# Kernel optimization log

Measured on AMD Instinct MI355X. Metric: run time of the kernel, lower is better.

## Reference

```python
import jax, jax.numpy as jnp
import numpy as np

B, S, D, H = 2, 2048, 1024, 16
DK = D // H


def setup_inputs() -> dict:
    key = jax.random.key(0)
    ks = jax.random.split(key, 11)
    scale = jnp.float32(1.0 / np.sqrt(D))
    inp = {
        "query": jax.random.normal(ks[0], (B, S, D), jnp.float32),
        "key": jax.random.normal(ks[1], (B, S, D), jnp.float32),
        "value": jax.random.normal(ks[2], (B, S, D), jnp.float32),
        # causal mask: True = masked (masked_fill semantics), broadcast over batch/heads
        "mask": jnp.triu(jnp.ones((S, S), dtype=bool), k=1)[None, None, :, :],
        "Wq": jax.random.normal(ks[3], (D, D), jnp.float32) * scale,
        "bq": jnp.zeros((D,), jnp.float32),
        "Wk": jax.random.normal(ks[4], (D, D), jnp.float32) * scale,
        "bk": jnp.zeros((D,), jnp.float32),
        "Wv": jax.random.normal(ks[5], (D, D), jnp.float32) * scale,
        "bv": jnp.zeros((D,), jnp.float32),
        "Wo": jax.random.normal(ks[6], (D, D), jnp.float32) * scale,
        "bo": jnp.zeros((D,), jnp.float32),
    }
    return inp


def _split_heads(x):
    # (B, S, D) -> (B, H, S, DK)
    b, s, _ = x.shape
    return x.reshape(b, s, H, DK).transpose(0, 2, 1, 3)


def reference(query, key, value, mask, Wq, bq, Wk, bk, Wv, bv, Wo, bo):
    # nn.Linear: y = x @ W.T + b
    q = _split_heads(query @ Wq.T + bq)
    k = _split_heads(key @ Wk.T + bk)
    v = _split_heads(value @ Wv.T + bv)

    inv_sqrt_dk = jnp.float32(1.0 / np.sqrt(DK))
    scores = jnp.einsum("bhqd,bhkd->bhqk", q, k) * inv_sqrt_dk  # (B,H,S,S)
    scores = jnp.where(mask, jnp.float32(-jnp.inf), scores)
    weights = jax.nn.softmax(scores, axis=-1)
    weights = jnp.nan_to_num(weights, nan=0.0)  # fully-masked rows -> 0

    attn = jnp.einsum("bhqk,bhkd->bhqd", weights, v)  # (B,H,S,DK)
    merged = attn.transpose(0, 2, 1, 3).reshape(B, S, D)  # merge heads
    return merged @ Wo.T + bo
```

## Files before the change

kernel.cpp:

```cpp
#include <hip/hip_runtime.h>


typedef unsigned short u16;
typedef unsigned int u32;
typedef __attribute__((ext_vector_type(8))) __bf16 bf16x8;
typedef __attribute__((ext_vector_type(8))) unsigned short us8;
typedef __attribute__((ext_vector_type(4))) unsigned short us4;
typedef __attribute__((ext_vector_type(4))) unsigned int u32x4;
typedef __attribute__((ext_vector_type(4))) float f32x4;

#define S_LEN 2048
#define D_DIM 1024
#define NH 16
#define DKH 64
#define Mi 1048576ULL

__device__ __forceinline__ u16 f2bf(float f) {
  return __builtin_bit_cast(u16, (__bf16)f);
}
__device__ __forceinline__ u32 pack2(float lo, float hi) {
  return (u32)f2bf(lo) | ((u32)f2bf(hi) << 16);
}
__device__ __forceinline__ bf16x8 ld_frag(const u16* p) {
  us8 v = *(const us8*)p;
  return __builtin_bit_cast(bf16x8, v);
}
__device__ __forceinline__ void gl2lds16(const u16* g, u16* l) {
  __builtin_amdgcn_global_load_lds(
      (__attribute__((address_space(1))) void*)(g),
      (__attribute__((address_space(3))) void*)(l), 16, 0, 0);
}
__device__ __forceinline__ void stage_f32(const float* __restrict__ g, int ld,
                                          u16* lds, int t) {
  int row = t >> 1, col = (t & 1) * 16;
  const float* p = g + (size_t)row * ld + col;
  us8 o0, o1;
  #pragma unroll
  for (int i = 0; i < 8; ++i) o0[i] = f2bf(p[i]);
  #pragma unroll
  for (int i = 0; i < 8; ++i) o1[i] = f2bf(p[8 + i]);
  *(us8*)&lds[row * 32 + col] = o0;
  *(us8*)&lds[row * 32 + col + 8] = o1;
}

__global__ __launch_bounds__(256, 1) void cvt_all(
    const float* __restrict__ q, const float* __restrict__ k, const float* __restrict__ v,
    const float* __restrict__ wq, const float* __restrict__ wk,
    const float* __restrict__ wv, const float* __restrict__ wo,
    u16* __restrict__ dst)
{
  size_t e0 = ((size_t)blockIdx.x * 256 + threadIdx.x) * 8;
  const float* s;
  if      (e0 <  4*Mi) s = q  + e0;
  else if (e0 <  8*Mi) s = k  + (e0 - 4*Mi);
  else if (e0 < 12*Mi) s = v  + (e0 - 8*Mi);
  else if (e0 < 13*Mi) s = wq + (e0 - 12*Mi);
  else if (e0 < 14*Mi) s = wk + (e0 - 13*Mi);
  else if (e0 < 15*Mi) s = wv + (e0 - 14*Mi);
  else                 s = wo + (e0 - 15*Mi);
  float4 a = ((const float4*)s)[0];
  float4 b = ((const float4*)s)[1];
  us8 o;
  o[0]=f2bf(a.x); o[1]=f2bf(a.y); o[2]=f2bf(a.z); o[3]=f2bf(a.w);
  o[4]=f2bf(b.x); o[5]=f2bf(b.y); o[6]=f2bf(b.z); o[7]=f2bf(b.w);
  *(us8*)(dst + e0) = o;
}

__global__ __launch_bounds__(256, 1) void gemm_qkv_bb(
    const u16* __restrict__ Aq, const u16* __restrict__ Ak, const u16* __restrict__ Av,
    const u16* __restrict__ Wqb, const u16* __restrict__ Wkb, const u16* __restrict__ Wvb,
    const float* __restrict__ bq, const float* __restrict__ bk, const float* __restrict__ bv,
    u16* __restrict__ Oq, u16* __restrict__ Ok, u16* __restrict__ Ov, float qscale)
{
  const int z = blockIdx.z;
  const u16* A = (z == 0) ? Aq : (z == 1) ? Ak : Av;
  const u16* W = (z == 0) ? Wqb : (z == 1) ? Wkb : Wvb;
  const float* bias = (z == 0) ? bq : (z == 1) ? bk : bv;
  u16* out = (z == 0) ? Oq : (z == 1) ? Ok : Ov;
  const float scale = (z == 0) ? qscale : 1.0f;
  const int K = 1024;

  __shared__ u16 lA[128 * 32];
  __shared__ u16 lB[128 * 32];
  const int t = threadIdx.x;
  const int w = t >> 6, l = t & 63;
  const int mblk = blockIdx.y * 128, nblk = blockIdx.x * 128;
  const int wm = (w & 1) * 64, wn = (w >> 1) * 64;
  const int lr = l & 15, lq = l >> 4;
  const int srow = l >> 2, scol = (l & 3) * 8;

  f32x4 acc[4][4] = {};

  for (int k0 = 0; k0 < K; k0 += 32) {
    __syncthreads();
    #pragma unroll
    for (int r = 0; r < 2; ++r) {
      int grp = r * 4 + w;
      gl2lds16(A + (size_t)(mblk + grp * 16 + srow) * K + k0 + scol, &lA[grp * 512]);
      gl2lds16(W + (size_t)(nblk + grp * 16 + srow) * K + k0 + scol, &lB[grp * 512]);
    }
    __syncthreads();
    bf16x8 aF[4], bF[4];
    #pragma unroll
    for (int mt = 0; mt < 4; ++mt)
      aF[mt] = ld_frag(&lA[(wm + mt * 16 + lr) * 32 + lq * 8]);
    #pragma unroll
    for (int nt = 0; nt < 4; ++nt)
      bF[nt] = ld_frag(&lB[(wn + nt * 16 + lr) * 32 + lq * 8]);
    #pragma unroll
    for (int mt = 0; mt < 4; ++mt)
      #pragma unroll
      for (int nt = 0; nt < 4; ++nt)
        acc[mt][nt] = __builtin_amdgcn_mfma_f32_16x16x32_bf16(aF[mt], bF[nt], acc[mt][nt], 0, 0, 0);
  }

  #pragma unroll
  for (int mt = 0; mt < 4; ++mt)
    #pragma unroll
    for (int nt = 0; nt < 4; ++nt)
      #pragma unroll
      for (int r = 0; r < 4; ++r) {
        int rowg = mblk + wm + mt * 16 + lq * 4 + r;
        int colg = nblk + wn + nt * 16 + lr;
        float v = (acc[mt][nt][r] + bias[colg]) * scale;
        int b = rowg >> 11, s = rowg & 2047;
        int h = colg >> 6, dk = colg & 63;
        if (z != 2)
          out[(((size_t)(b * NH + h)) * S_LEN + s) * DKH + dk] = f2bf(v);
        else
          out[(((size_t)(b * NH + h)) * DKH + dk) * S_LEN + s] = f2bf(v);
      }
}

__global__ __launch_bounds__(256, 1) void gemm_out_bb(
    const u16* __restrict__ A, const u16* __restrict__ W,
    const float* __restrict__ bias, float* __restrict__ out)
{
  const int K = 1024;
  __shared__ u16 lA[128 * 32];
  __shared__ u16 lB[128 * 32];
  const int t = threadIdx.x;
  const int w = t >> 6, l = t & 63;
  const int mblk = blockIdx.y * 128, nblk = blockIdx.x * 128;
  const int wm = (w & 1) * 64, wn = (w >> 1) * 64;
  const int lr = l & 15, lq = l >> 4;
  const int srow = l >> 2, scol = (l & 3) * 8;

  f32x4 acc[4][4] = {};

  for (int k0 = 0; k0 < K; k0 += 32) {
    __syncthreads();
    #pragma unroll
    for (int r = 0; r < 2; ++r) {
      int grp = r * 4 + w;
      gl2lds16(A + (size_t)(mblk + grp * 16 + srow) * K + k0 + scol, &lA[grp * 512]);
      gl2lds16(W + (size_t)(nblk + grp * 16 + srow) * K + k0 + scol, &lB[grp * 512]);
    }
    __syncthreads();
    bf16x8 aF[4], bF[4];
    #pragma unroll
    for (int mt = 0; mt < 4; ++mt)
      aF[mt] = ld_frag(&lA[(wm + mt * 16 + lr) * 32 + lq * 8]);
    #pragma unroll
    for (int nt = 0; nt < 4; ++nt)
      bF[nt] = ld_frag(&lB[(wn + nt * 16 + lr) * 32 + lq * 8]);
    #pragma unroll
    for (int mt = 0; mt < 4; ++mt)
      #pragma unroll
      for (int nt = 0; nt < 4; ++nt)
        acc[mt][nt] = __builtin_amdgcn_mfma_f32_16x16x32_bf16(aF[mt], bF[nt], acc[mt][nt], 0, 0, 0);
  }

  #pragma unroll
  for (int mt = 0; mt < 4; ++mt)
    #pragma unroll
    for (int nt = 0; nt < 4; ++nt)
      #pragma unroll
      for (int r = 0; r < 4; ++r) {
        int rowg = mblk + wm + mt * 16 + lq * 4 + r;
        int colg = nblk + wn + nt * 16 + lr;
        out[(size_t)rowg * D_DIM + colg] = acc[mt][nt][r] + bias[colg];
      }
}

__global__ __launch_bounds__(256, 1) void attn_fused(
    const u16* __restrict__ Q, const u16* __restrict__ K,
    const u16* __restrict__ Vt, u16* __restrict__ O)
{
  __shared__ u16 lK[2][64 * 64];
  __shared__ u16 lV[2][64 * 64];
  __shared__ u32 lPT[4 * 16 * 32];

  const int idx = blockIdx.x;
  const int s_ = idx >> 8;
  const int r_ = idx & 255;
  const int bh = r_ & 31;
  const int t_ = r_ >> 5;
  const int qt = (s_ == 0) ? t_ : (s_ == 1) ? 31 - t_ : (s_ == 2) ? 8 + t_ : 23 - t_;
  const int b = bh >> 4, h = bh & 15;
  const int t = threadIdx.x;
  const int w = t >> 6, l = t & 63;
  const int lr = l & 15, lq = l >> 4;

  const u16* Qp = Q + (size_t)bh * S_LEN * DKH;
  const u16* Kp = K + (size_t)bh * S_LEN * DKH;
  const u16* Vp = Vt + (size_t)bh * DKH * S_LEN;

  const int srow8 = l >> 3;
  const int schunk = l & 7;

  const int qrow = qt * 64 + w * 16 + lr;
  bf16x8 qf[2];
  qf[0] = ld_frag(Qp + (size_t)qrow * DKH + lq * 8);
  qf[1] = ld_frag(Qp + (size_t)qrow * DKH + 32 + lq * 8);

  f32x4 o[4] = {};
  f32x4 li4 = {};

  u32* pw = &lPT[w * 16 * 32];
  const int pswz = (lr & 7) << 2;

  #pragma unroll
  for (int r2 = 0; r2 < 2; ++r2) {
    int grp = r2 * 4 + w;
    int row = grp * 8 + srow8;
    int c = schunk ^ (row & 7);
    gl2lds16(Kp + (size_t)row * DKH + c * 8, &lK[0][grp * 512]);
    gl2lds16(Vp + (size_t)row * S_LEN + c * 8, &lV[0][grp * 512]);
  }

  for (int kt = 0; kt <= qt; ++kt) {
    const int cur = kt & 1;
    __syncthreads();

    if (kt < qt) {
      #pragma unroll
      for (int r2 = 0; r2 < 2; ++r2) {
        int grp = r2 * 4 + w;
        int row = grp * 8 + srow8;
        int c = schunk ^ (row & 7);
        gl2lds16(Kp + (size_t)((kt + 1) * 64 + row) * DKH + c * 8, &lK[cur ^ 1][grp * 512]);
        gl2lds16(Vp + (size_t)row * S_LEN + (kt + 1) * 64 + c * 8, &lV[cur ^ 1][grp * 512]);
      }
    }

    f32x4 st[4] = {};
    #pragma unroll
    for (int ks = 0; ks < 2; ++ks)
      #pragma unroll
      for (int nt = 0; nt < 4; ++nt) {
        int row = nt * 16 + lr;
        int cs = (ks * 4 + lq) ^ (row & 7);
        bf16x8 kb = ld_frag(&lK[cur][row * 64 + cs * 8]);
        st[nt] = __builtin_amdgcn_mfma_f32_16x16x32_bf16(kb, qf[ks], st[nt], 0, 0, 0);
      }

    float p[4][4];
    const bool diag = (kt == qt);
    const int qloc = w * 16 + lr;
    #pragma unroll
    for (int nt = 0; nt < 4; ++nt) {
      #pragma unroll
      for (int r = 0; r < 4; ++r) {
        int kk = nt * 16 + lq * 4 + r;
        float e = exp2f(st[nt][r]);
        p[nt][r] = (diag && kk > qloc) ? 0.0f : e;
        li4[r] += p[nt][r];
      }
    }

    #pragma unroll
    for (int nt = 0; nt < 4; ++nt) {
      #pragma unroll
      for (int i = 0; i < 2; ++i) {
        int pr = nt * 8 + lq * 2 + i;
        pw[lr * 32 + (pr ^ pswz)] = pack2(p[nt][2 * i], p[nt][2 * i + 1]);
      }
    }
    #pragma unroll
    for (int ks = 0; ks < 2; ++ks) {
      u32x4 pv;
      #pragma unroll
      for (int u = 0; u < 4; ++u) {
        int pr = ks * 16 + lq * 4 + u;
        pv[u] = pw[lr * 32 + (pr ^ pswz)];
      }
      bf16x8 pb = __builtin_bit_cast(bf16x8, pv);
      #pragma unroll
      for (int nt = 0; nt < 4; ++nt) {
        int vrow = nt * 16 + lr;
        int vcs = (ks * 4 + lq) ^ (vrow & 7);
        bf16x8 vb = ld_frag(&lV[cur][vrow * 64 + vcs * 8]);
        o[nt] = __builtin_amdgcn_mfma_f32_16x16x32_bf16(vb, pb, o[nt], 0, 0, 0);
      }
    }
  }

  float li = li4[0] + li4[1] + li4[2] + li4[3];
  li += __shfl_xor(li, 16);
  li += __shfl_xor(li, 32);
  const float rinv = 1.0f / li;

  const size_t orow = ((size_t)b * S_LEN + qt * 64 + w * 16 + lr) * D_DIM + h * DKH;
  #pragma unroll
  for (int nt = 0; nt < 4; ++nt) {
    us4 pk;
    #pragma unroll
    for (int r = 0; r < 4; ++r) pk[r] = f2bf(o[nt][r] * rinv);
    *(us4*)(O + orow + nt * 16 + lq * 4) = pk;
  }
}

extern "C" void kernel_launch(void* const* d_in, const int* in_sizes, int n_in,
                              void* d_out, int out_size, void* d_ws, size_t ws_size,
                              hipStream_t stream) {
  const float* query = (const float*)d_in[0];
  const float* key   = (const float*)d_in[1];
  const float* value = (const float*)d_in[2];
  const float* Wq = (const float*)d_in[4];
  const float* bq = (const float*)d_in[5];
  const float* Wk = (const float*)d_in[6];
  const float* bk = (const float*)d_in[7];
  const float* Wv = (const float*)d_in[8];
  const float* bv = (const float*)d_in[9];
  const float* Wo = (const float*)d_in[10];
  const float* bo = (const float*)d_in[11];
  float* out = (float*)d_out;

  const float qscale = 0.125f * 1.44269504088896341f;
  dim3 blk(256);

  u16* base = (u16*)d_ws;
  u16* Qb = base;
  u16* Kb = base + 4 * Mi;
  u16* Vb = base + 8 * Mi;

  u16* cvt = base + 12 * Mi;
  u16* qbf = cvt;
  u16* kbf = cvt + 4 * Mi;
  u16* vbf = cvt + 8 * Mi;
  u16* wqb = cvt + 12 * Mi;
  u16* wkb = cvt + 13 * Mi;
  u16* wvb = cvt + 14 * Mi;
  u16* wob = cvt + 15 * Mi;
  u16* Ab  = qbf;

  cvt_all<<<dim3(8192), blk, 0, stream>>>(query, key, value, Wq, Wk, Wv, Wo, cvt);
  gemm_qkv_bb<<<dim3(8, 32, 3), blk, 0, stream>>>(qbf, kbf, vbf, wqb, wkb, wvb,
                                                  bq, bk, bv, Qb, Kb, Vb, qscale);
  attn_fused<<<dim3(1024), blk, 0, stream>>>(Qb, Kb, Vb, Ab);
  gemm_out_bb<<<dim3(8, 32), blk, 0, stream>>>(Ab, wob, bo, out);
}
```

Before: 239.5 us.

## Keep softmax probabilities in registers via permuted K rows; narrow output GEMM tiles

The attention kernel permutes which K rows each lane reads, so the score MFMA output already matches the A-operand layout needed for the P·V MFMA. This removes the per-tile round trip of probabilities through shared memory, and the swizzle pattern is changed to match the new access order. The output projection GEMM moves to 128x64 tiles, doubling the grid to 512 blocks for better CU occupancy on the 1024-wide output, at the cost of more reloads of the A operand. The attention output is now written as scattered 2-byte stores instead of 8-byte vector stores, which may reduce store efficiency.

```diff
diff --git a/kernel.cpp b/kernel.cpp
--- a/kernel.cpp
+++ b/kernel.cpp
@@ -5,8 +5,6 @@
 typedef unsigned int u32;
 typedef __attribute__((ext_vector_type(8))) __bf16 bf16x8;
 typedef __attribute__((ext_vector_type(8))) unsigned short us8;
-typedef __attribute__((ext_vector_type(4))) unsigned short us4;
-typedef __attribute__((ext_vector_type(4))) unsigned int u32x4;
 typedef __attribute__((ext_vector_type(4))) float f32x4;
 
 #define S_LEN 2048
@@ -18,9 +16,6 @@
 __device__ __forceinline__ u16 f2bf(float f) {
   return __builtin_bit_cast(u16, (__bf16)f);
 }
-__device__ __forceinline__ u32 pack2(float lo, float hi) {
-  return (u32)f2bf(lo) | ((u32)f2bf(hi) << 16);
-}
 __device__ __forceinline__ bf16x8 ld_frag(const u16* p) {
   us8 v = *(const us8*)p;
   return __builtin_bit_cast(bf16x8, v);
@@ -29,18 +24,6 @@
   __builtin_amdgcn_global_load_lds(
       (__attribute__((address_space(1))) void*)(g),
       (__attribute__((address_space(3))) void*)(l), 16, 0, 0);
-}
-__device__ __forceinline__ void stage_f32(const float* __restrict__ g, int ld,
-                                          u16* lds, int t) {
-  int row = t >> 1, col = (t & 1) * 16;
-  const float* p = g + (size_t)row * ld + col;
-  us8 o0, o1;
-  #pragma unroll
-  for (int i = 0; i < 8; ++i) o0[i] = f2bf(p[i]);
-  #pragma unroll
-  for (int i = 0; i < 8; ++i) o1[i] = f2bf(p[8 + i]);
-  *(us8*)&lds[row * 32 + col] = o0;
-  *(us8*)&lds[row * 32 + col + 8] = o1;
 }
 
 __global__ __launch_bounds__(256, 1) void cvt_all(
@@ -138,15 +121,15 @@
 {
   const int K = 1024;
   __shared__ u16 lA[128 * 32];
-  __shared__ u16 lB[128 * 32];
+  __shared__ u16 lB[64 * 32];
   const int t = threadIdx.x;
   const int w = t >> 6, l = t & 63;
-  const int mblk = blockIdx.y * 128, nblk = blockIdx.x * 128;
-  const int wm = (w & 1) * 64, wn = (w >> 1) * 64;
+  const int mblk = blockIdx.y * 128, nblk = blockIdx.x * 64;
+  const int wm = (w & 1) * 64, wn = (w >> 1) * 32;
   const int lr = l & 15, lq = l >> 4;
   const int srow = l >> 2, scol = (l & 3) * 8;
 
-  f32x4 acc[4][4] = {};
+  f32x4 acc[4][2] = {};
 
   for (int k0 = 0; k0 < K; k0 += 32) {
     __syncthreads();
@@ -154,27 +137,27 @@
     for (int r = 0; r < 2; ++r) {
       int grp = r * 4 + w;
       gl2lds16(A + (size_t)(mblk + grp * 16 + srow) * K + k0 + scol, &lA[grp * 512]);
-      gl2lds16(W + (size_t)(nblk + grp * 16 + srow) * K + k0 + scol, &lB[grp * 512]);
     }
-    __syncthreads();
-    bf16x8 aF[4], bF[4];
+    gl2lds16(W + (size_t)(nblk + w * 16 + srow) * K + k0 + scol, &lB[w * 512]);
+    __syncthreads();
+    bf16x8 aF[4], bF[2];
     #pragma unroll
     for (int mt = 0; mt < 4; ++mt)
       aF[mt] = ld_frag(&lA[(wm + mt * 16 + lr) * 32 + lq * 8]);
     #pragma unroll
-    for (int nt = 0; nt < 4; ++nt)
+    for (int nt = 0; nt < 2; ++nt)
       bF[nt] = ld_frag(&lB[(wn + nt * 16 + lr) * 32 + lq * 8]);
     #pragma unroll
     for (int mt = 0; mt < 4; ++mt)
       #pragma unroll
-      for (int nt = 0; nt < 4; ++nt)
+      for (int nt = 0; nt < 2; ++nt)
         acc[mt][nt] = __builtin_amdgcn_mfma_f32_16x16x32_bf16(aF[mt], bF[nt], acc[mt][nt], 0, 0, 0);
   }
 
   #pragma unroll
   for (int mt = 0; mt < 4; ++mt)
     #pragma unroll
-    for (int nt = 0; nt < 4; ++nt)
+    for (int nt = 0; nt < 2; ++nt)
       #pragma unroll
       for (int r = 0; r < 4; ++r) {
         int rowg = mblk + wm + mt * 16 + lq * 4 + r;
@@ -189,7 +172,6 @@
 {
   __shared__ u16 lK[2][64 * 64];
   __shared__ u16 lV[2][64 * 64];
-  __shared__ u32 lPT[4 * 16 * 32];
 
   const int idx = blockIdx.x;
   const int s_ = idx >> 8;
@@ -217,14 +199,12 @@
   f32x4 o[4] = {};
   f32x4 li4 = {};
 
-  u32* pw = &lPT[w * 16 * 32];
-  const int pswz = (lr & 7) << 2;
-
   #pragma unroll
   for (int r2 = 0; r2 < 2; ++r2) {
     int grp = r2 * 4 + w;
     int row = grp * 8 + srow8;
-    int c = schunk ^ (row & 7);
+    int sw = (row & 3) | (((row >> 3) & 1) << 2);
+    int c = schunk ^ sw;
     gl2lds16(Kp + (size_t)row * DKH + c * 8, &lK[0][grp * 512]);
     gl2lds16(Vp + (size_t)row * S_LEN + c * 8, &lV[0][grp * 512]);
   }
@@ -238,7 +218,8 @@
       for (int r2 = 0; r2 < 2; ++r2) {
         int grp = r2 * 4 + w;
         int row = grp * 8 + srow8;
-        int c = schunk ^ (row & 7);
+        int sw = (row & 3) | (((row >> 3) & 1) << 2);
+        int c = schunk ^ sw;
         gl2lds16(Kp + (size_t)((kt + 1) * 64 + row) * DKH + c * 8, &lK[cur ^ 1][grp * 512]);
         gl2lds16(Vp + (size_t)row * S_LEN + (kt + 1) * 64 + c * 8, &lV[cur ^ 1][grp * 512]);
       }
@@ -246,52 +227,44 @@
 
     f32x4 st[4] = {};
     #pragma unroll
-    for (int ks = 0; ks < 2; ++ks)
+    for (int ksd = 0; ksd < 2; ++ksd)
       #pragma unroll
       for (int nt = 0; nt < 4; ++nt) {
-        int row = nt * 16 + lr;
-        int cs = (ks * 4 + lq) ^ (row & 7);
-        bf16x8 kb = ld_frag(&lK[cur][row * 64 + cs * 8]);
-        st[nt] = __builtin_amdgcn_mfma_f32_16x16x32_bf16(kb, qf[ks], st[nt], 0, 0, 0);
+        int sig = 32 * (nt >> 1) + 8 * (lr >> 2) + 4 * (nt & 1) + (lr & 3);
+        int slot = (ksd * 4 + lq) ^ (lr & 7);
+        bf16x8 kb = ld_frag(&lK[cur][sig * 64 + slot * 8]);
+        st[nt] = __builtin_amdgcn_mfma_f32_16x16x32_bf16(kb, qf[ksd], st[nt], 0, 0, 0);
       }
 
     float p[4][4];
     const bool diag = (kt == qt);
     const int qloc = w * 16 + lr;
     #pragma unroll
-    for (int nt = 0; nt < 4; ++nt) {
+    for (int nt = 0; nt < 4; ++nt)
       #pragma unroll
       for (int r = 0; r < 4; ++r) {
-        int kk = nt * 16 + lq * 4 + r;
+        int kk = 32 * (nt >> 1) + 8 * lq + 4 * (nt & 1) + r;
         float e = exp2f(st[nt][r]);
         p[nt][r] = (diag && kk > qloc) ? 0.0f : e;
         li4[r] += p[nt][r];
       }
-    }
-
-    #pragma unroll
-    for (int nt = 0; nt < 4; ++nt) {
-      #pragma unroll
-      for (int i = 0; i < 2; ++i) {
-        int pr = nt * 8 + lq * 2 + i;
-        pw[lr * 32 + (pr ^ pswz)] = pack2(p[nt][2 * i], p[nt][2 * i + 1]);
-      }
-    }
+
     #pragma unroll
     for (int ks = 0; ks < 2; ++ks) {
-      u32x4 pv;
-      #pragma unroll
-      for (int u = 0; u < 4; ++u) {
-        int pr = ks * 16 + lq * 4 + u;
-        pv[u] = pw[lr * 32 + (pr ^ pswz)];
-      }
-      bf16x8 pb = __builtin_bit_cast(bf16x8, pv);
-      #pragma unroll
-      for (int nt = 0; nt < 4; ++nt) {
-        int vrow = nt * 16 + lr;
-        int vcs = (ks * 4 + lq) ^ (vrow & 7);
-        bf16x8 vb = ld_frag(&lV[cur][vrow * 64 + vcs * 8]);
-        o[nt] = __builtin_amdgcn_mfma_f32_16x16x32_bf16(vb, pb, o[nt], 0, 0, 0);
+      us8 av;
+      #pragma unroll
+      for (int j = 0; j < 4; ++j) {
+        av[j] = f2bf(p[2 * ks][j]);
+        av[4 + j] = f2bf(p[2 * ks + 1][j]);
+      }
+      bf16x8 pa = __builtin_bit_cast(bf16x8, av);
+      #pragma unroll
+      for (int dblk = 0; dblk < 4; ++dblk) {
+        int d = dblk * 16 + lr;
+        int sw = (d & 3) | (((d >> 3) & 1) << 2);
+        int slot = (4 * ks + lq) ^ sw;
+        bf16x8 vb = ld_frag(&lV[cur][d * 64 + slot * 8]);
+        o[dblk] = __builtin_amdgcn_mfma_f32_16x16x32_bf16(pa, vb, o[dblk], 0, 0, 0);
       }
     }
   }
@@ -299,16 +272,16 @@
   float li = li4[0] + li4[1] + li4[2] + li4[3];
   li += __shfl_xor(li, 16);
   li += __shfl_xor(li, 32);
-  const float rinv = 1.0f / li;
-
-  const size_t orow = ((size_t)b * S_LEN + qt * 64 + w * 16 + lr) * D_DIM + h * DKH;
-  #pragma unroll
-  for (int nt = 0; nt < 4; ++nt) {
-    us4 pk;
-    #pragma unroll
-    for (int r = 0; r < 4; ++r) pk[r] = f2bf(o[nt][r] * rinv);
-    *(us4*)(O + orow + nt * 16 + lq * 4) = pk;
-  }
+  float ri[4];
+  #pragma unroll
+  for (int r = 0; r < 4; ++r) ri[r] = 1.0f / __shfl(li, lq * 4 + r);
+
+  const size_t obase = ((size_t)b * S_LEN + qt * 64 + w * 16) * D_DIM + h * DKH;
+  #pragma unroll
+  for (int dblk = 0; dblk < 4; ++dblk)
+    #pragma unroll
+    for (int r = 0; r < 4; ++r)
+      O[obase + (size_t)(lq * 4 + r) * D_DIM + dblk * 16 + lr] = f2bf(o[dblk][r] * ri[r]);
 }
 
 extern "C" void kernel_launch(void* const* d_in, const int* in_sizes, int n_in,
@@ -349,5 +322,5 @@
   gemm_qkv_bb<<<dim3(8, 32, 3), blk, 0, stream>>>(qbf, kbf, vbf, wqb, wkb, wvb,
                                                   bq, bk, bv, Qb, Kb, Vb, qscale);
   attn_fused<<<dim3(1024), blk, 0, stream>>>(Qb, Kb, Vb, Ab);
-  gemm_out_bb<<<dim3(8, 32), blk, 0, stream>>>(Ab, wob, bo, out);
-}
+  gemm_out_bb<<<dim3(16, 32), blk, 0, stream>>>(Ab, wob, bo, out);
+}
```

New measurement: 233.5 us. 2.5% less time.
